# Kernel tuning notes

Measured on AMD Instinct MI355X. Metric: run time of the kernel, lower is better.

Reference implementation:

```python
import jax, jax.numpy as jnp
import numpy as np
from jax import lax

INPUT_SIZE, HIDDEN, LAYERS, OUT = 49, 32, 2, 10
B, T = 512, 1024


def _param(key, shape, fan):
    bound = 1.0 / np.sqrt(fan)
    return jax.random.uniform(key, shape, jnp.float32, -bound, bound)


def setup_inputs() -> dict:
    key = jax.random.key(0)
    ks = jax.random.split(key, 12)
    return {
        "x": jax.random.normal(ks[0], (B, T, INPUT_SIZE), jnp.float32),
        "W_ih0": _param(ks[1], (4 * HIDDEN, INPUT_SIZE), HIDDEN),
        "W_hh0": _param(ks[2], (4 * HIDDEN, HIDDEN), HIDDEN),
        "b_ih0": _param(ks[3], (4 * HIDDEN,), HIDDEN),
        "b_hh0": _param(ks[4], (4 * HIDDEN,), HIDDEN),
        "W_ih1": _param(ks[5], (4 * HIDDEN, HIDDEN), HIDDEN),
        "W_hh1": _param(ks[6], (4 * HIDDEN, HIDDEN), HIDDEN),
        "b_ih1": _param(ks[7], (4 * HIDDEN,), HIDDEN),
        "b_hh1": _param(ks[8], (4 * HIDDEN,), HIDDEN),
        "W_out": _param(ks[9], (OUT, HIDDEN), HIDDEN),
        "b_out": _param(ks[10], (OUT,), HIDDEN),
    }


def _lstm_layer(x_tbd, W_ih, W_hh, b_ih, b_hh):
    # x_tbd: [T, B, D]; PyTorch gate order i, f, g, o stacked along 4H.
    H = W_hh.shape[1]
    # Precompute input contribution for all timesteps in one GEMM.
    xg = jnp.einsum('tbd,gd->tbg', x_tbd, W_ih) + b_ih + b_hh  # [T, B, 4H]

    def step(carry, xg_t):
        h, c = carry
        gates = xg_t + h @ W_hh.T  # [B, 4H]
        i, f, g, o = jnp.split(gates, 4, axis=-1)
        i = jax.nn.sigmoid(i)
        f = jax.nn.sigmoid(f)
        g = jnp.tanh(g)
        o = jax.nn.sigmoid(o)
        c = f * c + i * g
        h = o * jnp.tanh(c)
        return (h, c), h

    Bsz = x_tbd.shape[1]
    init = (jnp.zeros((Bsz, H), x_tbd.dtype), jnp.zeros((Bsz, H), x_tbd.dtype))
    _, hs = lax.scan(step, init, xg)
    return hs  # [T, B, H]


def reference(x, W_ih0, W_hh0, b_ih0, b_hh0, W_ih1, W_hh1, b_ih1, b_hh1, W_out, b_out):
    # Eval-mode forward (inter-layer dropout disabled).
    xt = jnp.transpose(x, (1, 0, 2))  # [T, B, 49]
    h0 = _lstm_layer(xt, W_ih0, W_hh0, b_ih0, b_hh0)  # [T, B, 32]
    h1 = _lstm_layer(h0, W_ih1, W_hh1, b_ih1, b_hh1)  # [T, B, 32]
    r_out = jnp.transpose(h1, (1, 0, 2))  # [B, T, 32]
    return r_out @ W_out.T + b_out  # [B, T, 10]
```

## Files before the change

kernel.cpp:

```cpp
#include <hip/hip_runtime.h>
#include <cstddef>

#define TSTEPS 1024
#define NIN    49
#define HID    32
#define OUTD   10
#define XSTR   52
#define SUPERS 259

typedef float v2f __attribute__((ext_vector_type(2)));

template<int CTRL>
__device__ __forceinline__ float quad(float v) {
    return __int_as_float(__builtin_amdgcn_mov_dpp(__float_as_int(v), CTRL, 0xF, 0xF, true));
}
__device__ __forceinline__ float sigm(float x) {
    return __builtin_amdgcn_rcpf(1.f + __expf(-x));
}
__device__ __forceinline__ void pkfma(v2f& acc, v2f a, v2f b) {
    asm("v_pk_fma_f32 %0, %1, %2, %0" : "+v"(acc) : "v"(a), "v"(b));
}

#define LOADH2(BASE, H2)                                                     \
    v2f H2[8];                                                               \
    {                                                                        \
        const float4* hp_ = (const float4*)(BASE);                           \
        const float4 a_ = hp_[0], b_ = hp_[1], c_ = hp_[2], d_ = hp_[3];     \
        H2[0] = (v2f){a_.x, a_.y}; H2[1] = (v2f){a_.z, a_.w};                \
        H2[2] = (v2f){b_.x, b_.y}; H2[3] = (v2f){b_.z, b_.w};                \
        H2[4] = (v2f){c_.x, c_.y}; H2[5] = (v2f){c_.z, c_.w};                \
        H2[6] = (v2f){d_.x, d_.y}; H2[7] = (v2f){d_.z, d_.w};                \
    }

#define DOTPK(W2, H2, S0, S1, S2, S3)                                        \
    float S0, S1, S2, S3;                                                    \
    {                                                                        \
        v2f p0 = {0.f,0.f}, p1 = {0.f,0.f}, p2 = {0.f,0.f}, p3 = {0.f,0.f}; \
        _Pragma("unroll")                                                    \
        for (int m_ = 0; m_ < 8; ++m_) {                                     \
            pkfma(p0, W2[0][m_], H2[m_]);                                    \
            pkfma(p1, W2[1][m_], H2[m_]);                                    \
            pkfma(p2, W2[2][m_], H2[m_]);                                    \
            pkfma(p3, W2[3][m_], H2[m_]);                                    \
        }                                                                    \
        S0 = p0.x + p0.y; S1 = p1.x + p1.y;                                  \
        S2 = p2.x + p2.y; S3 = p3.x + p3.y;                                  \
        S0 += quad<0xB1>(S0); S1 += quad<0xB1>(S1);                          \
        S2 += quad<0xB1>(S2); S3 += quad<0xB1>(S3);                          \
    }

__device__ __forceinline__ float gate_act(float s0, float s1, float s2, float s3,
                                          int gp, float& c) {
    const float inA = gp ? s2 + s2 : s0;
    const float inB = gp ? s3 : s1;
    const float sA = sigm(inA);
    const float sB = sigm(inB);
    const float vA = gp ? fmaf(2.f, sA, -1.f) : sA;
    const float xA = quad<0xB1>(vA);
    const float xB = quad<0xB1>(sB);
    const float ig = gp ? xA : vA;
    const float fg = gp ? xB : sB;
    const float gg = gp ? vA : xA;
    const float og = gp ? sB : xB;
    c = fmaf(fg, c, ig * gg);
    return og * fmaf(2.f, sigm(c + c), -1.f);
}

extern "C" __global__ void __launch_bounds__(256, 2)
lstm_pk4(const float* __restrict__ x,
         const float* __restrict__ Wih0, const float* __restrict__ Whh0,
         const float* __restrict__ bih0, const float* __restrict__ bhh0,
         const float* __restrict__ Wih1, const float* __restrict__ Whh1,
         const float* __restrict__ bih1, const float* __restrict__ bhh1,
         const float* __restrict__ Wout, const float* __restrict__ bout,
         float* __restrict__ y)
{
    const int tid  = threadIdx.x;
    const int wv   = tid >> 6;
    const int lane = tid & 63;

    __shared__ float xs[2 * 16 * XSTR];
    __shared__ float xg0[16][HID][4];
    __shared__ float xg1[16][HID][4];
    __shared__ float h0r[16][HID];
    __shared__ float h1r[16][HID];

    {
        float* z0 = &h0r[0][0];
        float* z1 = &h1r[0][0];
        for (int i = tid; i < 16 * HID; i += 256) { z0[i] = 0.f; z1[i] = 0.f; }
    }

    const float* __restrict__ xb = x + (size_t)blockIdx.x * TSTEPS * NIN;
    float* __restrict__ yb       = y + (size_t)blockIdx.x * TSTEPS * OUTD;

    if (wv == 0) {
        const int j = lane >> 1, gp = lane & 1;
        v2f wh0[4][8];
#pragma unroll
        for (int g = 0; g < 4; ++g) {
            const float* wr = Whh0 + (g * HID + j) * HID + 16 * gp;
#pragma unroll
            for (int m = 0; m < 8; ++m) wh0[g][m] = (v2f){wr[2*m], wr[2*m + 1]};
        }
        float c0 = 0.f;
        __builtin_amdgcn_s_setprio(1);
        __syncthreads();
        __syncthreads();
        for (int s = 0; s < SUPERS; ++s) {
            if (s < 256) {
#pragma unroll
                for (int u = 0; u < 4; ++u) {
                    const int t = 4 * s + u;
                    LOADH2(&h0r[(t + 15) & 15][16 * gp], hv)
                    DOTPK(wh0, hv, s0, s1, s2, s3)
                    const float4 xg = *(const float4*)&xg0[t & 15][j][0];
                    const float hval = gate_act(s0 + xg.x, s1 + xg.y,
                                                s2 + xg.z, s3 + xg.w, gp, c0);
                    if (gp == 0) h0r[t & 15][j] = hval;
                }
            }
            __syncthreads();
        }
    } else if (wv == 1) {
        const int j = lane >> 1, gp = lane & 1;
        v2f wi1[4][8];
        float b1v[4];
#pragma unroll
        for (int g = 0; g < 4; ++g) {
            const float* wr = Wih1 + (g * HID + j) * HID + 16 * gp;
#pragma unroll
            for (int m = 0; m < 8; ++m) wi1[g][m] = (v2f){wr[2*m], wr[2*m + 1]};
            b1v[g] = bih1[g * HID + j] + bhh1[g * HID + j];
        }
        float wo[8], bo = 0.f;
        const int po = lane >> 2, kq = lane & 3;
        if (lane < 40) {
#pragma unroll
            for (int m = 0; m < 8; ++m) wo[m] = Wout[po * HID + kq * 8 + m];
            bo = bout[po];
        } else {
#pragma unroll
            for (int m = 0; m < 8; ++m) wo[m] = 0.f;
        }
        __syncthreads();
        __syncthreads();
        for (int s = 0; s < SUPERS; ++s) {
            if (s >= 1 && s <= 256) {
#pragma unroll
                for (int u = 0; u < 4; ++u) {
                    const int t = 4 * (s - 1) + u;
                    LOADH2(&h0r[t & 15][16 * gp], hv)
                    DOTPK(wi1, hv, s0, s1, s2, s3)
                    if (gp == 0) {
                        float4 o;
                        o.x = s0 + b1v[0]; o.y = s1 + b1v[1];
                        o.z = s2 + b1v[2]; o.w = s3 + b1v[3];
                        *(float4*)&xg1[t & 15][j][0] = o;
                    }
                }
            }
            if (s >= 3) {
#pragma unroll
                for (int u = 0; u < 4; ++u) {
                    const int ty = 4 * (s - 3) + u;
                    const float* hb = &h1r[ty & 15][kq * 8];
                    const float4 va = *(const float4*)hb;
                    const float4 vb = *(const float4*)(hb + 4);
                    float acc = wo[0]*va.x + wo[1]*va.y + wo[2]*va.z + wo[3]*va.w
                              + wo[4]*vb.x + wo[5]*vb.y + wo[6]*vb.z + wo[7]*vb.w;
                    acc += quad<0xB1>(acc);
                    acc += quad<0x4E>(acc);
                    if (lane < 40 && kq == 0) yb[(size_t)ty * OUTD + po] = acc + bo;
                }
            }
            __syncthreads();
        }
    } else if (wv == 2) {
        const int j = lane >> 1, gp = lane & 1;
        v2f wh1[4][8];
#pragma unroll
        for (int g = 0; g < 4; ++g) {
            const float* wr = Whh1 + (g * HID + j) * HID + 16 * gp;
#pragma unroll
            for (int m = 0; m < 8; ++m) wh1[g][m] = (v2f){wr[2*m], wr[2*m + 1]};
        }
        float c1 = 0.f;
        __builtin_amdgcn_s_setprio(1);
        __syncthreads();
        __syncthreads();
        for (int s = 0; s < SUPERS; ++s) {
            if (s >= 2 && s <= 257) {
#pragma unroll
                for (int u = 0; u < 4; ++u) {
                    const int t = 4 * (s - 2) + u;
                    LOADH2(&h1r[(t + 15) & 15][16 * gp], hv)
                    DOTPK(wh1, hv, s0, s1, s2, s3)
                    const float4 xg = *(const float4*)&xg1[t & 15][j][0];
                    const float hval = gate_act(s0 + xg.x, s1 + xg.y,
                                                s2 + xg.z, s3 + xg.w, gp, c1);
                    if (gp == 0) h1r[t & 15][j] = hval;
                }
            }
            __syncthreads();
        }
    } else {
        const int jj = lane & 31;
        const int gA = lane >> 5;
        const int gB = 2 + (lane >> 5);

        v2f wa2[24], wb2[24];
        float wa48, wb48, b0a, b0b;
        {
            const float* wra = Wih0 + (gA * HID + jj) * NIN;
            const float* wrb = Wih0 + (gB * HID + jj) * NIN;
#pragma unroll
            for (int m = 0; m < 24; ++m) {
                wa2[m] = (v2f){wra[2*m], wra[2*m + 1]};
                wb2[m] = (v2f){wrb[2*m], wrb[2*m + 1]};
            }
            wa48 = wra[48]; wb48 = wrb[48];
            b0a = bih0[gA * HID + jj] + bhh0[gA * HID + jj];
            b0b = bih0[gB * HID + jj] + bhh0[gB * HID + jj];
        }

        int laddr[13];
#pragma unroll
        for (int r = 0; r < 13; ++r) {
            const int idx = lane + r * 64;
            const int s_  = idx / NIN;
            laddr[r] = s_ * XSTR + (idx - s_ * NIN);
        }
        float xr[13];

        auto issue = [&](int cn) {
            const float* src = xb + (size_t)cn * 16 * NIN;
#pragma unroll
            for (int r = 0; r < 12; ++r) xr[r] = src[lane + r * 64];
            if (lane < 16) xr[12] = src[lane + 768];
        };
        auto drain = [&](int cn) {
            float* dst = &xs[(cn & 1) * (16 * XSTR)];
#pragma unroll
            for (int r = 0; r < 12; ++r) dst[laddr[r]] = xr[r];
            if (lane < 16) dst[laddr[12]] = xr[12];
        };
        auto pdot = [&](int t) {
            const float* xp = &xs[((t >> 4) & 1) * (16 * XSTR) + (t & 15) * XSTR];
            const float4* x4 = (const float4*)xp;
            v2f aA0 = (v2f){b0a, 0.f}, aA1 = (v2f){0.f, 0.f};
            v2f aB0 = (v2f){b0b, 0.f}, aB1 = (v2f){0.f, 0.f};
#pragma unroll
            for (int u = 0; u < 12; ++u) {
                const float4 xv = x4[u];
                const v2f xlo = (v2f){xv.x, xv.y};
                const v2f xhi = (v2f){xv.z, xv.w};
                pkfma(aA0, wa2[2*u],     xlo);
                pkfma(aA1, wa2[2*u + 1], xhi);
                pkfma(aB0, wb2[2*u],     xlo);
                pkfma(aB1, wb2[2*u + 1], xhi);
            }
            const float x48 = xp[48];
            const float a0 = fmaf(wa48, x48, (aA0.x + aA0.y) + (aA1.x + aA1.y));
            const float a2 = fmaf(wb48, x48, (aB0.x + aB0.y) + (aB1.x + aB1.y));
            xg0[t & 15][jj][gA] = a0;
            xg0[t & 15][jj][gB] = a2;
        };

        issue(0);
        drain(0);
        __syncthreads();
        pdot(0); pdot(1); pdot(2); pdot(3);
        __syncthreads();

        for (int s = 0; s < SUPERS; ++s) {
            if (s < 255) {
                const int cn = (s >> 2) + 1;
                if ((s & 3) == 0 && cn < 64) issue(cn);
                pdot(4 * s + 4); pdot(4 * s + 5); pdot(4 * s + 6); pdot(4 * s + 7);
                if ((s & 3) == 2 && cn < 64) drain(cn);
            }
            __syncthreads();
        }
    }
}

extern "C" void kernel_launch(void* const* d_in, const int* in_sizes, int n_in,
                              void* d_out, int out_size, void* d_ws, size_t ws_size,
                              hipStream_t stream) {
    (void)in_sizes; (void)n_in; (void)d_ws; (void)ws_size; (void)out_size;
    const float* x    = (const float*)d_in[0];
    const float* Wih0 = (const float*)d_in[1];
    const float* Whh0 = (const float*)d_in[2];
    const float* bih0 = (const float*)d_in[3];
    const float* bhh0 = (const float*)d_in[4];
    const float* Wih1 = (const float*)d_in[5];
    const float* Whh1 = (const float*)d_in[6];
    const float* bih1 = (const float*)d_in[7];
    const float* bhh1 = (const float*)d_in[8];
    const float* Wout = (const float*)d_in[9];
    const float* bout = (const float*)d_in[10];
    float* y = (float*)d_out;

    lstm_pk4<<<dim3(512), dim3(256), 0, stream>>>(
        x, Wih0, Whh0, bih0, bhh0, Wih1, Whh1, bih1, bhh1, Wout, bout, y);
}
```

Measured before the change: 400.4 us.

## Process two batch sequences per block to interleave independent recurrences

Each block now handles two batch rows instead of one. Every wave runs both recurrences side by side, so the independent dot products and gate activations can fill each other's latency on the serial critical path. The grid halves to 256 blocks and launch bounds drop to one block per SIMD group, so the GPU gets fewer blocks and lower occupancy. Register pressure roughly doubles for the x staging buffers and accumulators.

```diff
diff --git a/kernel.cpp b/kernel.cpp
--- a/kernel.cpp
+++ b/kernel.cpp
@@ -7,6 +7,7 @@
 #define OUTD   10
 #define XSTR   52
 #define SUPERS 259
+#define NB     2
 
 typedef float v2f __attribute__((ext_vector_type(2)));
 
@@ -32,21 +33,26 @@
         H2[6] = (v2f){d_.x, d_.y}; H2[7] = (v2f){d_.z, d_.w};                \
     }
 
-#define DOTPK(W2, H2, S0, S1, S2, S3)                                        \
-    float S0, S1, S2, S3;                                                    \
+#define DOTPK2(W2, HA, HB, A0,A1,A2,A3, B0,B1,B2,B3)                         \
+    float A0,A1,A2,A3,B0,B1,B2,B3;                                           \
     {                                                                        \
-        v2f p0 = {0.f,0.f}, p1 = {0.f,0.f}, p2 = {0.f,0.f}, p3 = {0.f,0.f}; \
+        v2f pa0={0.f,0.f}, pa1={0.f,0.f}, pa2={0.f,0.f}, pa3={0.f,0.f};      \
+        v2f pb0={0.f,0.f}, pb1={0.f,0.f}, pb2={0.f,0.f}, pb3={0.f,0.f};      \
         _Pragma("unroll")                                                    \
         for (int m_ = 0; m_ < 8; ++m_) {                                     \
-            pkfma(p0, W2[0][m_], H2[m_]);                                    \
-            pkfma(p1, W2[1][m_], H2[m_]);                                    \
-            pkfma(p2, W2[2][m_], H2[m_]);                                    \
-            pkfma(p3, W2[3][m_], H2[m_]);                                    \
+            pkfma(pa0, W2[0][m_], HA[m_]); pkfma(pb0, W2[0][m_], HB[m_]);    \
+            pkfma(pa1, W2[1][m_], HA[m_]); pkfma(pb1, W2[1][m_], HB[m_]);    \
+            pkfma(pa2, W2[2][m_], HA[m_]); pkfma(pb2, W2[2][m_], HB[m_]);    \
+            pkfma(pa3, W2[3][m_], HA[m_]); pkfma(pb3, W2[3][m_], HB[m_]);    \
         }                                                                    \
-        S0 = p0.x + p0.y; S1 = p1.x + p1.y;                                  \
-        S2 = p2.x + p2.y; S3 = p3.x + p3.y;                                  \
-        S0 += quad<0xB1>(S0); S1 += quad<0xB1>(S1);                          \
-        S2 += quad<0xB1>(S2); S3 += quad<0xB1>(S3);                          \
+        A0 = pa0.x + pa0.y; A1 = pa1.x + pa1.y;                              \
+        A2 = pa2.x + pa2.y; A3 = pa3.x + pa3.y;                              \
+        B0 = pb0.x + pb0.y; B1 = pb1.x + pb1.y;                              \
+        B2 = pb2.x + pb2.y; B3 = pb3.x + pb3.y;                              \
+        A0 += quad<0xB1>(A0); A1 += quad<0xB1>(A1);                          \
+        A2 += quad<0xB1>(A2); A3 += quad<0xB1>(A3);                          \
+        B0 += quad<0xB1>(B0); B1 += quad<0xB1>(B1);                          \
+        B2 += quad<0xB1>(B2); B3 += quad<0xB1>(B3);                          \
     }
 
 __device__ __forceinline__ float gate_act(float s0, float s1, float s2, float s3,
@@ -66,33 +72,35 @@
     return og * fmaf(2.f, sigm(c + c), -1.f);
 }
 
-extern "C" __global__ void __launch_bounds__(256, 2)
-lstm_pk4(const float* __restrict__ x,
-         const float* __restrict__ Wih0, const float* __restrict__ Whh0,
-         const float* __restrict__ bih0, const float* __restrict__ bhh0,
-         const float* __restrict__ Wih1, const float* __restrict__ Whh1,
-         const float* __restrict__ bih1, const float* __restrict__ bhh1,
-         const float* __restrict__ Wout, const float* __restrict__ bout,
-         float* __restrict__ y)
+extern "C" __global__ void __launch_bounds__(256, 1)
+lstm_pk4x2(const float* __restrict__ x,
+           const float* __restrict__ Wih0, const float* __restrict__ Whh0,
+           const float* __restrict__ bih0, const float* __restrict__ bhh0,
+           const float* __restrict__ Wih1, const float* __restrict__ Whh1,
+           const float* __restrict__ bih1, const float* __restrict__ bhh1,
+           const float* __restrict__ Wout, const float* __restrict__ bout,
+           float* __restrict__ y)
 {
     const int tid  = threadIdx.x;
     const int wv   = tid >> 6;
     const int lane = tid & 63;
 
-    __shared__ float xs[2 * 16 * XSTR];
-    __shared__ float xg0[16][HID][4];
-    __shared__ float xg1[16][HID][4];
-    __shared__ float h0r[16][HID];
-    __shared__ float h1r[16][HID];
+    __shared__ __align__(16) float xs[NB][2 * 16 * XSTR];
+    __shared__ __align__(16) float xg0[NB][16][HID][4];
+    __shared__ __align__(16) float xg1[NB][16][HID][4];
+    __shared__ __align__(16) float h0r[NB][16][HID];
+    __shared__ __align__(16) float h1r[NB][16][HID];
 
     {
-        float* z0 = &h0r[0][0];
-        float* z1 = &h1r[0][0];
-        for (int i = tid; i < 16 * HID; i += 256) { z0[i] = 0.f; z1[i] = 0.f; }
+        float* z0 = &h0r[0][0][0];
+        float* z1 = &h1r[0][0][0];
+        for (int i = tid; i < NB * 16 * HID; i += 256) { z0[i] = 0.f; z1[i] = 0.f; }
     }
 
-    const float* __restrict__ xb = x + (size_t)blockIdx.x * TSTEPS * NIN;
-    float* __restrict__ yb       = y + (size_t)blockIdx.x * TSTEPS * OUTD;
+    const float* __restrict__ xb0 = x + (size_t)blockIdx.x * NB * TSTEPS * NIN;
+    const float* __restrict__ xb1 = xb0 + TSTEPS * NIN;
+    float* __restrict__ yb0      = y + (size_t)blockIdx.x * NB * TSTEPS * OUTD;
+    float* __restrict__ yb1      = yb0 + TSTEPS * OUTD;
 
     if (wv == 0) {
         const int j = lane >> 1, gp = lane & 1;
@@ -103,7 +111,7 @@
 #pragma unroll
             for (int m = 0; m < 8; ++m) wh0[g][m] = (v2f){wr[2*m], wr[2*m + 1]};
         }
-        float c0 = 0.f;
+        float ca = 0.f, cb = 0.f;
         __builtin_amdgcn_s_setprio(1);
         __syncthreads();
         __syncthreads();
@@ -112,12 +120,19 @@
 #pragma unroll
                 for (int u = 0; u < 4; ++u) {
                     const int t = 4 * s + u;
-                    LOADH2(&h0r[(t + 15) & 15][16 * gp], hv)
-                    DOTPK(wh0, hv, s0, s1, s2, s3)
-                    const float4 xg = *(const float4*)&xg0[t & 15][j][0];
-                    const float hval = gate_act(s0 + xg.x, s1 + xg.y,
-                                                s2 + xg.z, s3 + xg.w, gp, c0);
-                    if (gp == 0) h0r[t & 15][j] = hval;
+                    LOADH2(&h0r[0][(t + 15) & 15][16 * gp], hva)
+                    LOADH2(&h0r[1][(t + 15) & 15][16 * gp], hvb)
+                    const float4 xga = *(const float4*)&xg0[0][t & 15][j][0];
+                    const float4 xgb = *(const float4*)&xg0[1][t & 15][j][0];
+                    DOTPK2(wh0, hva, hvb, a0, a1, a2, a3, b0, b1, b2, b3)
+                    const float ha = gate_act(a0 + xga.x, a1 + xga.y,
+                                              a2 + xga.z, a3 + xga.w, gp, ca);
+                    const float hb = gate_act(b0 + xgb.x, b1 + xgb.y,
+                                              b2 + xgb.z, b3 + xgb.w, gp, cb);
+                    if (gp == 0) {
+                        h0r[0][t & 15][j] = ha;
+                        h0r[1][t & 15][j] = hb;
+                    }
                 }
             }
             __syncthreads();
@@ -150,13 +165,17 @@
 #pragma unroll
                 for (int u = 0; u < 4; ++u) {
                     const int t = 4 * (s - 1) + u;
-                    LOADH2(&h0r[t & 15][16 * gp], hv)
-                    DOTPK(wi1, hv, s0, s1, s2, s3)
+                    LOADH2(&h0r[0][t & 15][16 * gp], hva)
+                    LOADH2(&h0r[1][t & 15][16 * gp], hvb)
+                    DOTPK2(wi1, hva, hvb, a0, a1, a2, a3, b0, b1, b2, b3)
                     if (gp == 0) {
-                        float4 o;
-                        o.x = s0 + b1v[0]; o.y = s1 + b1v[1];
-                        o.z = s2 + b1v[2]; o.w = s3 + b1v[3];
-                        *(float4*)&xg1[t & 15][j][0] = o;
+                        float4 oa, ob;
+                        oa.x = a0 + b1v[0]; oa.y = a1 + b1v[1];
+                        oa.z = a2 + b1v[2]; oa.w = a3 + b1v[3];
+                        ob.x = b0 + b1v[0]; ob.y = b1 + b1v[1];
+                        ob.z = b2 + b1v[2]; ob.w = b3 + b1v[3];
+                        *(float4*)&xg1[0][t & 15][j][0] = oa;
+                        *(float4*)&xg1[1][t & 15][j][0] = ob;
                     }
                 }
             }
@@ -164,14 +183,26 @@
 #pragma unroll
                 for (int u = 0; u < 4; ++u) {
                     const int ty = 4 * (s - 3) + u;
-                    const float* hb = &h1r[ty & 15][kq * 8];
-                    const float4 va = *(const float4*)hb;
-                    const float4 vb = *(const float4*)(hb + 4);
-                    float acc = wo[0]*va.x + wo[1]*va.y + wo[2]*va.z + wo[3]*va.w
-                              + wo[4]*vb.x + wo[5]*vb.y + wo[6]*vb.z + wo[7]*vb.w;
-                    acc += quad<0xB1>(acc);
-                    acc += quad<0x4E>(acc);
-                    if (lane < 40 && kq == 0) yb[(size_t)ty * OUTD + po] = acc + bo;
+                    {
+                        const float* hb = &h1r[0][ty & 15][kq * 8];
+                        const float4 va = *(const float4*)hb;
+                        const float4 vb = *(const float4*)(hb + 4);
+                        float acc = wo[0]*va.x + wo[1]*va.y + wo[2]*va.z + wo[3]*va.w
+                                  + wo[4]*vb.x + wo[5]*vb.y + wo[6]*vb.z + wo[7]*vb.w;
+                        acc += quad<0xB1>(acc);
+                        acc += quad<0x4E>(acc);
+                        if (lane < 40 && kq == 0) yb0[(size_t)ty * OUTD + po] = acc + bo;
+                    }
+                    {
+                        const float* hb = &h1r[1][ty & 15][kq * 8];
+                        const float4 va = *(const float4*)hb;
+                        const float4 vb = *(const float4*)(hb + 4);
+                        float acc = wo[0]*va.x + wo[1]*va.y + wo[2]*va.z + wo[3]*va.w
+                                  + wo[4]*vb.x + wo[5]*vb.y + wo[6]*vb.z + wo[7]*vb.w;
+                        acc += quad<0xB1>(acc);
+                        acc += quad<0x4E>(acc);
+                        if (lane < 40 && kq == 0) yb1[(size_t)ty * OUTD + po] = acc + bo;
+                    }
                 }
             }
             __syncthreads();
@@ -185,7 +216,7 @@
 #pragma unroll
             for (int m = 0; m < 8; ++m) wh1[g][m] = (v2f){wr[2*m], wr[2*m + 1]};
         }
-        float c1 = 0.f;
+        float ca = 0.f, cb = 0.f;
         __builtin_amdgcn_s_setprio(1);
         __syncthreads();
         __syncthreads();
@@ -194,12 +225,19 @@
 #pragma unroll
                 for (int u = 0; u < 4; ++u) {
                     const int t = 4 * (s - 2) + u;
-                    LOADH2(&h1r[(t + 15) & 15][16 * gp], hv)
-                    DOTPK(wh1, hv, s0, s1, s2, s3)
-                    const float4 xg = *(const float4*)&xg1[t & 15][j][0];
-                    const float hval = gate_act(s0 + xg.x, s1 + xg.y,
-                                                s2 + xg.z, s3 + xg.w, gp, c1);
-                    if (gp == 0) h1r[t & 15][j] = hval;
+                    LOADH2(&h1r[0][(t + 15) & 15][16 * gp], hva)
+                    LOADH2(&h1r[1][(t + 15) & 15][16 * gp], hvb)
+                    const float4 xga = *(const float4*)&xg1[0][t & 15][j][0];
+                    const float4 xgb = *(const float4*)&xg1[1][t & 15][j][0];
+                    DOTPK2(wh1, hva, hvb, a0, a1, a2, a3, b0, b1, b2, b3)
+                    const float ha = gate_act(a0 + xga.x, a1 + xga.y,
+                                              a2 + xga.z, a3 + xga.w, gp, ca);
+                    const float hb = gate_act(b0 + xgb.x, b1 + xgb.y,
+                                              b2 + xgb.z, b3 + xgb.w, gp, cb);
+                    if (gp == 0) {
+                        h1r[0][t & 15][j] = ha;
+                        h1r[1][t & 15][j] = hb;
+                    }
                 }
             }
             __syncthreads();
@@ -231,22 +269,30 @@
             const int s_  = idx / NIN;
             laddr[r] = s_ * XSTR + (idx - s_ * NIN);
         }
-        float xr[13];
+        float xra[13], xrb[13];
 
         auto issue = [&](int cn) {
-            const float* src = xb + (size_t)cn * 16 * NIN;
-#pragma unroll
-            for (int r = 0; r < 12; ++r) xr[r] = src[lane + r * 64];
-            if (lane < 16) xr[12] = src[lane + 768];
+            const float* sa = xb0 + (size_t)cn * 16 * NIN;
+            const float* sb = xb1 + (size_t)cn * 16 * NIN;
+#pragma unroll
+            for (int r = 0; r < 12; ++r) {
+                xra[r] = sa[lane + r * 64];
+                xrb[r] = sb[lane + r * 64];
+            }
+            if (lane < 16) { xra[12] = sa[lane + 768]; xrb[12] = sb[lane + 768]; }
         };
         auto drain = [&](int cn) {
-            float* dst = &xs[(cn & 1) * (16 * XSTR)];
-#pragma unroll
-            for (int r = 0; r < 12; ++r) dst[laddr[r]] = xr[r];
-            if (lane < 16) dst[laddr[12]] = xr[12];
+            float* da = &xs[0][(cn & 1) * (16 * XSTR)];
+            float* db = &xs[1][(cn & 1) * (16 * XSTR)];
+#pragma unroll
+            for (int r = 0; r < 12; ++r) {
+                da[laddr[r]] = xra[r];
+                db[laddr[r]] = xrb[r];
+            }
+            if (lane < 16) { da[laddr[12]] = xra[12]; db[laddr[12]] = xrb[12]; }
         };
-        auto pdot = [&](int t) {
-            const float* xp = &xs[((t >> 4) & 1) * (16 * XSTR) + (t & 15) * XSTR];
+        auto pdot1 = [&](int t, int b) {
+            const float* xp = &xs[b][((t >> 4) & 1) * (16 * XSTR) + (t & 15) * XSTR];
             const float4* x4 = (const float4*)xp;
             v2f aA0 = (v2f){b0a, 0.f}, aA1 = (v2f){0.f, 0.f};
             v2f aB0 = (v2f){b0b, 0.f}, aB1 = (v2f){0.f, 0.f};
@@ -263,21 +309,25 @@
             const float x48 = xp[48];
             const float a0 = fmaf(wa48, x48, (aA0.x + aA0.y) + (aA1.x + aA1.y));
             const float a2 = fmaf(wb48, x48, (aB0.x + aB0.y) + (aB1.x + aB1.y));
-            xg0[t & 15][jj][gA] = a0;
-            xg0[t & 15][jj][gB] = a2;
+            xg0[b][t & 15][jj][gA] = a0;
+            xg0[b][t & 15][jj][gB] = a2;
         };
 
         issue(0);
         drain(0);
         __syncthreads();
-        pdot(0); pdot(1); pdot(2); pdot(3);
+        pdot1(0, 0); pdot1(0, 1); pdot1(1, 0); pdot1(1, 1);
+        pdot1(2, 0); pdot1(2, 1); pdot1(3, 0); pdot1(3, 1);
         __syncthreads();
 
         for (int s = 0; s < SUPERS; ++s) {
             if (s < 255) {
                 const int cn = (s >> 2) + 1;
                 if ((s & 3) == 0 && cn < 64) issue(cn);
-                pdot(4 * s + 4); pdot(4 * s + 5); pdot(4 * s + 6); pdot(4 * s + 7);
+                pdot1(4 * s + 4, 0); pdot1(4 * s + 4, 1);
+                pdot1(4 * s + 5, 0); pdot1(4 * s + 5, 1);
+                pdot1(4 * s + 6, 0); pdot1(4 * s + 6, 1);
+                pdot1(4 * s + 7, 0); pdot1(4 * s + 7, 1);
                 if ((s & 3) == 2 && cn < 64) drain(cn);
             }
             __syncthreads();
@@ -302,6 +352,6 @@
     const float* bout = (const float*)d_in[10];
     float* y = (float*)d_out;
 
-    lstm_pk4<<<dim3(512), dim3(256), 0, stream>>>(
+    lstm_pk4x2<<<dim3(512 / NB), dim3(256), 0, stream>>>(
         x, Wih0, Whh0, bih0, bhh0, Wih1, Whh1, bih1, bhh1, Wout, bout, y);
 }
```

Result: slower. 546.4 us (+36.5%).

## Fuse LSTM wave roles into two waves per block with interleaved work

Applied to the files above, without the earlier changes.

Merges the four specialized waves into two. One wave runs the layer-0 recurrence, the layer-1 input projection and the output projection. The other runs the layer-0 input projection and the layer-1 recurrence. In steady state the independent work is interleaved within each timestep so it can fill the latency gaps of the serial recurrence, and the block shrinks to 128 threads. The risk is a longer per-wave instruction stream on the critical path, plus the loss of the priority boost that was previously given to the recurrence waves.

```diff
diff --git a/kernel.cpp b/kernel.cpp
--- a/kernel.cpp
+++ b/kernel.cpp
@@ -66,29 +66,29 @@
     return og * fmaf(2.f, sigm(c + c), -1.f);
 }
 
-extern "C" __global__ void __launch_bounds__(256, 2)
-lstm_pk4(const float* __restrict__ x,
-         const float* __restrict__ Wih0, const float* __restrict__ Whh0,
-         const float* __restrict__ bih0, const float* __restrict__ bhh0,
-         const float* __restrict__ Wih1, const float* __restrict__ Whh1,
-         const float* __restrict__ bih1, const float* __restrict__ bhh1,
-         const float* __restrict__ Wout, const float* __restrict__ bout,
-         float* __restrict__ y)
+extern "C" __global__ void __launch_bounds__(128, 2)
+lstm_fuse2(const float* __restrict__ x,
+           const float* __restrict__ Wih0, const float* __restrict__ Whh0,
+           const float* __restrict__ bih0, const float* __restrict__ bhh0,
+           const float* __restrict__ Wih1, const float* __restrict__ Whh1,
+           const float* __restrict__ bih1, const float* __restrict__ bhh1,
+           const float* __restrict__ Wout, const float* __restrict__ bout,
+           float* __restrict__ y)
 {
     const int tid  = threadIdx.x;
     const int wv   = tid >> 6;
     const int lane = tid & 63;
 
-    __shared__ float xs[2 * 16 * XSTR];
-    __shared__ float xg0[16][HID][4];
-    __shared__ float xg1[16][HID][4];
-    __shared__ float h0r[16][HID];
-    __shared__ float h1r[16][HID];
+    __shared__ __align__(16) float xs[2 * 16 * XSTR];
+    __shared__ __align__(16) float xg0[16][HID][4];
+    __shared__ __align__(16) float xg1[16][HID][4];
+    __shared__ __align__(16) float h0r[16][HID];
+    __shared__ __align__(16) float h1r[16][HID];
 
     {
         float* z0 = &h0r[0][0];
         float* z1 = &h1r[0][0];
-        for (int i = tid; i < 16 * HID; i += 256) { z0[i] = 0.f; z1[i] = 0.f; }
+        for (int i = tid; i < 16 * HID; i += 128) { z0[i] = 0.f; z1[i] = 0.f; }
     }
 
     const float* __restrict__ xb = x + (size_t)blockIdx.x * TSTEPS * NIN;
@@ -96,74 +96,52 @@
 
     if (wv == 0) {
         const int j = lane >> 1, gp = lane & 1;
-        v2f wh0[4][8];
+        v2f wh0[4][8], wi1[4][8];
+        float b1v[4];
 #pragma unroll
         for (int g = 0; g < 4; ++g) {
-            const float* wr = Whh0 + (g * HID + j) * HID + 16 * gp;
-#pragma unroll
-            for (int m = 0; m < 8; ++m) wh0[g][m] = (v2f){wr[2*m], wr[2*m + 1]};
+            const float* wr0 = Whh0 + (g * HID + j) * HID + 16 * gp;
+            const float* wr1 = Wih1 + (g * HID + j) * HID + 16 * gp;
+#pragma unroll
+            for (int m = 0; m < 8; ++m) {
+                wh0[g][m] = (v2f){wr0[2*m], wr0[2*m + 1]};
+                wi1[g][m] = (v2f){wr1[2*m], wr1[2*m + 1]};
+            }
+            b1v[g] = bih1[g * HID + j] + bhh1[g * HID + j];
+        }
+        float wo[8], bo = 0.f;
+        const int po = lane >> 2, kq = lane & 3;
+        if (lane < 40) {
+#pragma unroll
+            for (int m = 0; m < 8; ++m) wo[m] = Wout[po * HID + kq * 8 + m];
+            bo = bout[po];
+        } else {
+#pragma unroll
+            for (int m = 0; m < 8; ++m) wo[m] = 0.f;
         }
         float c0 = 0.f;
-        __builtin_amdgcn_s_setprio(1);
         __syncthreads();
         __syncthreads();
         for (int s = 0; s < SUPERS; ++s) {
-            if (s < 256) {
+            if (s >= 3 && s < 256) {
 #pragma unroll
                 for (int u = 0; u < 4; ++u) {
                     const int t = 4 * s + u;
+                    LOADH2(&h0r[(t - 4) & 15][16 * gp], hq)
                     LOADH2(&h0r[(t + 15) & 15][16 * gp], hv)
+                    const float4 xg = *(const float4*)&xg0[t & 15][j][0];
                     DOTPK(wh0, hv, s0, s1, s2, s3)
-                    const float4 xg = *(const float4*)&xg0[t & 15][j][0];
+                    DOTPK(wi1, hq, q0, q1, q2, q3)
                     const float hval = gate_act(s0 + xg.x, s1 + xg.y,
                                                 s2 + xg.z, s3 + xg.w, gp, c0);
-                    if (gp == 0) h0r[t & 15][j] = hval;
-                }
-            }
-            __syncthreads();
-        }
-    } else if (wv == 1) {
-        const int j = lane >> 1, gp = lane & 1;
-        v2f wi1[4][8];
-        float b1v[4];
-#pragma unroll
-        for (int g = 0; g < 4; ++g) {
-            const float* wr = Wih1 + (g * HID + j) * HID + 16 * gp;
-#pragma unroll
-            for (int m = 0; m < 8; ++m) wi1[g][m] = (v2f){wr[2*m], wr[2*m + 1]};
-            b1v[g] = bih1[g * HID + j] + bhh1[g * HID + j];
-        }
-        float wo[8], bo = 0.f;
-        const int po = lane >> 2, kq = lane & 3;
-        if (lane < 40) {
-#pragma unroll
-            for (int m = 0; m < 8; ++m) wo[m] = Wout[po * HID + kq * 8 + m];
-            bo = bout[po];
-        } else {
-#pragma unroll
-            for (int m = 0; m < 8; ++m) wo[m] = 0.f;
-        }
-        __syncthreads();
-        __syncthreads();
-        for (int s = 0; s < SUPERS; ++s) {
-            if (s >= 1 && s <= 256) {
-#pragma unroll
-                for (int u = 0; u < 4; ++u) {
-                    const int t = 4 * (s - 1) + u;
-                    LOADH2(&h0r[t & 15][16 * gp], hv)
-                    DOTPK(wi1, hv, s0, s1, s2, s3)
                     if (gp == 0) {
+                        h0r[t & 15][j] = hval;
                         float4 o;
-                        o.x = s0 + b1v[0]; o.y = s1 + b1v[1];
-                        o.z = s2 + b1v[2]; o.w = s3 + b1v[3];
-                        *(float4*)&xg1[t & 15][j][0] = o;
-                    }
-                }
-            }
-            if (s >= 3) {
-#pragma unroll
-                for (int u = 0; u < 4; ++u) {
-                    const int ty = 4 * (s - 3) + u;
+                        o.x = q0 + b1v[0]; o.y = q1 + b1v[1];
+                        o.z = q2 + b1v[2]; o.w = q3 + b1v[3];
+                        *(float4*)&xg1[(t - 4) & 15][j][0] = o;
+                    }
+                    const int ty = t - 12;
                     const float* hb = &h1r[ty & 15][kq * 8];
                     const float4 va = *(const float4*)hb;
                     const float4 vb = *(const float4*)(hb + 4);
@@ -173,10 +151,51 @@
                     acc += quad<0x4E>(acc);
                     if (lane < 40 && kq == 0) yb[(size_t)ty * OUTD + po] = acc + bo;
                 }
+            } else {
+                if (s < 256) {
+#pragma unroll
+                    for (int u = 0; u < 4; ++u) {
+                        const int t = 4 * s + u;
+                        LOADH2(&h0r[(t + 15) & 15][16 * gp], hv)
+                        DOTPK(wh0, hv, s0, s1, s2, s3)
+                        const float4 xg = *(const float4*)&xg0[t & 15][j][0];
+                        const float hval = gate_act(s0 + xg.x, s1 + xg.y,
+                                                    s2 + xg.z, s3 + xg.w, gp, c0);
+                        if (gp == 0) h0r[t & 15][j] = hval;
+                    }
+                }
+                if (s >= 1 && s <= 256) {
+#pragma unroll
+                    for (int u = 0; u < 4; ++u) {
+                        const int tq = 4 * (s - 1) + u;
+                        LOADH2(&h0r[tq & 15][16 * gp], hq)
+                        DOTPK(wi1, hq, q0, q1, q2, q3)
+                        if (gp == 0) {
+                            float4 o;
+                            o.x = q0 + b1v[0]; o.y = q1 + b1v[1];
+                            o.z = q2 + b1v[2]; o.w = q3 + b1v[3];
+                            *(float4*)&xg1[tq & 15][j][0] = o;
+                        }
+                    }
+                }
+                if (s >= 3) {
+#pragma unroll
+                    for (int u = 0; u < 4; ++u) {
+                        const int ty = 4 * (s - 3) + u;
+                        const float* hb = &h1r[ty & 15][kq * 8];
+                        const float4 va = *(const float4*)hb;
+                        const float4 vb = *(const float4*)(hb + 4);
+                        float acc = wo[0]*va.x + wo[1]*va.y + wo[2]*va.z + wo[3]*va.w
+                                  + wo[4]*vb.x + wo[5]*vb.y + wo[6]*vb.z + wo[7]*vb.w;
+                        acc += quad<0xB1>(acc);
+                        acc += quad<0x4E>(acc);
+                        if (lane < 40 && kq == 0) yb[(size_t)ty * OUTD + po] = acc + bo;
+                    }
+                }
             }
             __syncthreads();
         }
-    } else if (wv == 2) {
+    } else {
         const int j = lane >> 1, gp = lane & 1;
         v2f wh1[4][8];
 #pragma unroll
@@ -185,30 +204,9 @@
 #pragma unroll
             for (int m = 0; m < 8; ++m) wh1[g][m] = (v2f){wr[2*m], wr[2*m + 1]};
         }
-        float c1 = 0.f;
-        __builtin_amdgcn_s_setprio(1);
-        __syncthreads();
-        __syncthreads();
-        for (int s = 0; s < SUPERS; ++s) {
-            if (s >= 2 && s <= 257) {
-#pragma unroll
-                for (int u = 0; u < 4; ++u) {
-                    const int t = 4 * (s - 2) + u;
-                    LOADH2(&h1r[(t + 15) & 15][16 * gp], hv)
-                    DOTPK(wh1, hv, s0, s1, s2, s3)
-                    const float4 xg = *(const float4*)&xg1[t & 15][j][0];
-                    const float hval = gate_act(s0 + xg.x, s1 + xg.y,
-                                                s2 + xg.z, s3 + xg.w, gp, c1);
-                    if (gp == 0) h1r[t & 15][j] = hval;
-                }
-            }
-            __syncthreads();
-        }
-    } else {
         const int jj = lane & 31;
         const int gA = lane >> 5;
         const int gB = 2 + (lane >> 5);
-
         v2f wa2[24], wb2[24];
         float wa48, wb48, b0a, b0b;
         {
@@ -267,6 +265,8 @@
             xg0[t & 15][jj][gB] = a2;
         };
 
+        float c1 = 0.f;
+
         issue(0);
         drain(0);
         __syncthreads();
@@ -274,11 +274,40 @@
         __syncthreads();
 
         for (int s = 0; s < SUPERS; ++s) {
-            if (s < 255) {
+            if (s >= 2 && s < 255) {
                 const int cn = (s >> 2) + 1;
                 if ((s & 3) == 0 && cn < 64) issue(cn);
-                pdot(4 * s + 4); pdot(4 * s + 5); pdot(4 * s + 6); pdot(4 * s + 7);
+#pragma unroll
+                for (int u = 0; u < 4; ++u) {
+                    const int t = 4 * (s - 2) + u;
+                    LOADH2(&h1r[(t + 15) & 15][16 * gp], hv)
+                    const float4 xg = *(const float4*)&xg1[t & 15][j][0];
+                    DOTPK(wh1, hv, s0, s1, s2, s3)
+                    const float hval = gate_act(s0 + xg.x, s1 + xg.y,
+                                                s2 + xg.z, s3 + xg.w, gp, c1);
+                    if (gp == 0) h1r[t & 15][j] = hval;
+                    pdot(4 * (s + 1) + u);
+                }
                 if ((s & 3) == 2 && cn < 64) drain(cn);
+            } else {
+                if (s < 255) {
+                    const int cn = (s >> 2) + 1;
+                    if ((s & 3) == 0 && cn < 64) issue(cn);
+                    pdot(4 * s + 4); pdot(4 * s + 5); pdot(4 * s + 6); pdot(4 * s + 7);
+                    if ((s & 3) == 2 && cn < 64) drain(cn);
+                }
+                if (s >= 2 && s <= 257) {
+#pragma unroll
+                    for (int u = 0; u < 4; ++u) {
+                        const int t = 4 * (s - 2) + u;
+                        LOADH2(&h1r[(t + 15) & 15][16 * gp], hv)
+                        const float4 xg = *(const float4*)&xg1[t & 15][j][0];
+                        DOTPK(wh1, hv, s0, s1, s2, s3)
+                        const float hval = gate_act(s0 + xg.x, s1 + xg.y,
+                                                    s2 + xg.z, s3 + xg.w, gp, c1);
+                        if (gp == 0) h1r[t & 15][j] = hval;
+                    }
+                }
             }
             __syncthreads();
         }
@@ -302,6 +331,6 @@
     const float* bout = (const float*)d_in[10];
     float* y = (float*)d_out;
 
-    lstm_pk4<<<dim3(512), dim3(256), 0, stream>>>(
+    lstm_fuse2<<<dim3(512), dim3(128), 0, stream>>>(
         x, Wih0, Whh0, bih0, bhh0, Wih1, Whh1, bih1, bhh1, Wout, bout, y);
 }
```

Measured after the change: 671.0 us. 67.6% more time.

## Replace block-wide barriers with per-stage LDS counter flags between warp roles

Applied to the files above, without the earlier changes.

Removes the lockstep __syncthreads per super-step and has each wavefront role (input projection, layer-0 recurrence, layer-1 input GEMM/output projection, layer-1 recurrence) publish progress through release-stores to shared counters, while consumers spin with acquire loads and s_sleep. This lets the stages drift within the 16-slot ring buffers so the slowest wave no longer stalls all four at every step. It adds polling overhead and relies on the ring-distance checks being correct for memory ordering.

```diff
diff --git a/kernel.cpp b/kernel.cpp
--- a/kernel.cpp
+++ b/kernel.cpp
@@ -6,7 +6,7 @@
 #define HID    32
 #define OUTD   10
 #define XSTR   52
-#define SUPERS 259
+#define NGRP   256
 
 typedef float v2f __attribute__((ext_vector_type(2)));
 
@@ -19,6 +19,20 @@
 }
 __device__ __forceinline__ void pkfma(v2f& acc, v2f a, v2f b) {
     asm("v_pk_fma_f32 %0, %1, %2, %0" : "+v"(acc) : "v"(a), "v"(b));
+}
+
+__device__ __forceinline__ int ldacq(const int* p) {
+    return __hip_atomic_load(p, __ATOMIC_ACQUIRE, __HIP_MEMORY_SCOPE_WORKGROUP);
+}
+__device__ __forceinline__ void pub(int* p, int v, int lane) {
+    if (lane == 0)
+        __hip_atomic_store(p, v, __ATOMIC_RELEASE, __HIP_MEMORY_SCOPE_WORKGROUP);
+}
+__device__ __forceinline__ void waitge(const int* p, int need, int& cache) {
+    if (cache >= need) return;
+    int c = ldacq(p);
+    while (c < need) { __builtin_amdgcn_s_sleep(1); c = ldacq(p); }
+    cache = c;
 }
 
 #define LOADH2(BASE, H2)                                                     \
@@ -67,29 +81,32 @@
 }
 
 extern "C" __global__ void __launch_bounds__(256, 2)
-lstm_pk4(const float* __restrict__ x,
-         const float* __restrict__ Wih0, const float* __restrict__ Whh0,
-         const float* __restrict__ bih0, const float* __restrict__ bhh0,
-         const float* __restrict__ Wih1, const float* __restrict__ Whh1,
-         const float* __restrict__ bih1, const float* __restrict__ bhh1,
-         const float* __restrict__ Wout, const float* __restrict__ bout,
-         float* __restrict__ y)
+lstm_async(const float* __restrict__ x,
+           const float* __restrict__ Wih0, const float* __restrict__ Whh0,
+           const float* __restrict__ bih0, const float* __restrict__ bhh0,
+           const float* __restrict__ Wih1, const float* __restrict__ Whh1,
+           const float* __restrict__ bih1, const float* __restrict__ bhh1,
+           const float* __restrict__ Wout, const float* __restrict__ bout,
+           float* __restrict__ y)
 {
     const int tid  = threadIdx.x;
     const int wv   = tid >> 6;
     const int lane = tid & 63;
 
-    __shared__ float xs[2 * 16 * XSTR];
-    __shared__ float xg0[16][HID][4];
-    __shared__ float xg1[16][HID][4];
-    __shared__ float h0r[16][HID];
-    __shared__ float h1r[16][HID];
+    __shared__ __align__(16) float xs[2 * 16 * XSTR];
+    __shared__ __align__(16) float xg0[16][HID][4];
+    __shared__ __align__(16) float xg1[16][HID][4];
+    __shared__ __align__(16) float h0r[16][HID];
+    __shared__ __align__(16) float h1r[16][HID];
+    __shared__ int ctr[5];
 
     {
         float* z0 = &h0r[0][0];
         float* z1 = &h1r[0][0];
         for (int i = tid; i < 16 * HID; i += 256) { z0[i] = 0.f; z1[i] = 0.f; }
+        if (tid < 5) ctr[tid] = -1;
     }
+    __syncthreads();
 
     const float* __restrict__ xb = x + (size_t)blockIdx.x * TSTEPS * NIN;
     float* __restrict__ yb       = y + (size_t)blockIdx.x * TSTEPS * OUTD;
@@ -104,23 +121,22 @@
             for (int m = 0; m < 8; ++m) wh0[g][m] = (v2f){wr[2*m], wr[2*m + 1]};
         }
         float c0 = 0.f;
+        int cProd = -1, cQd = -1;
         __builtin_amdgcn_s_setprio(1);
-        __syncthreads();
-        __syncthreads();
-        for (int s = 0; s < SUPERS; ++s) {
-            if (s < 256) {
-#pragma unroll
-                for (int u = 0; u < 4; ++u) {
-                    const int t = 4 * s + u;
-                    LOADH2(&h0r[(t + 15) & 15][16 * gp], hv)
-                    DOTPK(wh0, hv, s0, s1, s2, s3)
-                    const float4 xg = *(const float4*)&xg0[t & 15][j][0];
-                    const float hval = gate_act(s0 + xg.x, s1 + xg.y,
-                                                s2 + xg.z, s3 + xg.w, gp, c0);
-                    if (gp == 0) h0r[t & 15][j] = hval;
-                }
-            }
-            __syncthreads();
+        for (int g = 0; g < NGRP; ++g) {
+            waitge(&ctr[0], 4 * g + 3, cProd);
+            if (g >= 4) waitge(&ctr[2], 4 * g - 13, cQd);
+#pragma unroll
+            for (int u = 0; u < 4; ++u) {
+                const int t = 4 * g + u;
+                LOADH2(&h0r[(t + 15) & 15][16 * gp], hv)
+                DOTPK(wh0, hv, s0, s1, s2, s3)
+                const float4 xg = *(const float4*)&xg0[t & 15][j][0];
+                const float hval = gate_act(s0 + xg.x, s1 + xg.y,
+                                            s2 + xg.z, s3 + xg.w, gp, c0);
+                if (gp == 0) h0r[t & 15][j] = hval;
+            }
+            pub(&ctr[1], 4 * g + 3, lane);
         }
     } else if (wv == 1) {
         const int j = lane >> 1, gp = lane & 1;
@@ -143,27 +159,31 @@
 #pragma unroll
             for (int m = 0; m < 8; ++m) wo[m] = 0.f;
         }
-        __syncthreads();
-        __syncthreads();
-        for (int s = 0; s < SUPERS; ++s) {
-            if (s >= 1 && s <= 256) {
+        int cL0 = -1, cL1b = -1, cL1d = -1;
+        for (int g = 0; g < NGRP + 2; ++g) {
+            if (g < NGRP) {
+                waitge(&ctr[1], 4 * g + 3, cL0);
+                if (g >= 4) waitge(&ctr[3], 4 * g - 13, cL1b);
 #pragma unroll
                 for (int u = 0; u < 4; ++u) {
-                    const int t = 4 * (s - 1) + u;
-                    LOADH2(&h0r[t & 15][16 * gp], hv)
-                    DOTPK(wi1, hv, s0, s1, s2, s3)
+                    const int t = 4 * g + u;
+                    LOADH2(&h0r[t & 15][16 * gp], hq)
+                    DOTPK(wi1, hq, q0, q1, q2, q3)
                     if (gp == 0) {
                         float4 o;
-                        o.x = s0 + b1v[0]; o.y = s1 + b1v[1];
-                        o.z = s2 + b1v[2]; o.w = s3 + b1v[3];
+                        o.x = q0 + b1v[0]; o.y = q1 + b1v[1];
+                        o.z = q2 + b1v[2]; o.w = q3 + b1v[3];
                         *(float4*)&xg1[t & 15][j][0] = o;
                     }
                 }
-            }
-            if (s >= 3) {
+                pub(&ctr[2], 4 * g + 3, lane);
+            }
+            if (g >= 2) {
+                const int gy = g - 2;
+                waitge(&ctr[3], 4 * gy + 3, cL1d);
 #pragma unroll
                 for (int u = 0; u < 4; ++u) {
-                    const int ty = 4 * (s - 3) + u;
+                    const int ty = 4 * gy + u;
                     const float* hb = &h1r[ty & 15][kq * 8];
                     const float4 va = *(const float4*)hb;
                     const float4 vb = *(const float4*)(hb + 4);
@@ -173,8 +193,8 @@
                     acc += quad<0x4E>(acc);
                     if (lane < 40 && kq == 0) yb[(size_t)ty * OUTD + po] = acc + bo;
                 }
-            }
-            __syncthreads();
+                pub(&ctr[4], 4 * gy + 3, lane);
+            }
         }
     } else if (wv == 2) {
         const int j = lane >> 1, gp = lane & 1;
@@ -186,23 +206,22 @@
             for (int m = 0; m < 8; ++m) wh1[g][m] = (v2f){wr[2*m], wr[2*m + 1]};
         }
         float c1 = 0.f;
+        int cQd = -1, cPrj = -1;
         __builtin_amdgcn_s_setprio(1);
-        __syncthreads();
-        __syncthreads();
-        for (int s = 0; s < SUPERS; ++s) {
-            if (s >= 2 && s <= 257) {
-#pragma unroll
-                for (int u = 0; u < 4; ++u) {
-                    const int t = 4 * (s - 2) + u;
-                    LOADH2(&h1r[(t + 15) & 15][16 * gp], hv)
-                    DOTPK(wh1, hv, s0, s1, s2, s3)
-                    const float4 xg = *(const float4*)&xg1[t & 15][j][0];
-                    const float hval = gate_act(s0 + xg.x, s1 + xg.y,
-                                                s2 + xg.z, s3 + xg.w, gp, c1);
-                    if (gp == 0) h1r[t & 15][j] = hval;
-                }
-            }
-            __syncthreads();
+        for (int g = 0; g < NGRP; ++g) {
+            waitge(&ctr[2], 4 * g + 3, cQd);
+            if (g >= 4) waitge(&ctr[4], 4 * g - 13, cPrj);
+#pragma unroll
+            for (int u = 0; u < 4; ++u) {
+                const int t = 4 * g + u;
+                LOADH2(&h1r[(t + 15) & 15][16 * gp], hv)
+                DOTPK(wh1, hv, s0, s1, s2, s3)
+                const float4 xg = *(const float4*)&xg1[t & 15][j][0];
+                const float hval = gate_act(s0 + xg.x, s1 + xg.y,
+                                            s2 + xg.z, s3 + xg.w, gp, c1);
+                if (gp == 0) h1r[t & 15][j] = hval;
+            }
+            pub(&ctr[3], 4 * g + 3, lane);
         }
     } else {
         const int jj = lane & 31;
@@ -269,18 +288,15 @@
 
         issue(0);
         drain(0);
-        __syncthreads();
-        pdot(0); pdot(1); pdot(2); pdot(3);
-        __syncthreads();
-
-        for (int s = 0; s < SUPERS; ++s) {
-            if (s < 255) {
-                const int cn = (s >> 2) + 1;
-                if ((s & 3) == 0 && cn < 64) issue(cn);
-                pdot(4 * s + 4); pdot(4 * s + 5); pdot(4 * s + 6); pdot(4 * s + 7);
-                if ((s & 3) == 2 && cn < 64) drain(cn);
-            }
-            __syncthreads();
+
+        int cL0 = -1;
+        for (int g = 0; g < NGRP; ++g) {
+            if (g >= 4) waitge(&ctr[1], 4 * g - 13, cL0);
+            const int cn = (g >> 2) + 1;
+            if ((g & 3) == 0 && cn < 64) issue(cn);
+            pdot(4 * g); pdot(4 * g + 1); pdot(4 * g + 2); pdot(4 * g + 3);
+            if ((g & 3) == 2 && cn < 64) drain(cn);
+            pub(&ctr[0], 4 * g + 3, lane);
         }
     }
 }
@@ -302,6 +318,6 @@
     const float* bout = (const float*)d_in[10];
     float* y = (float*)d_out;
 
-    lstm_pk4<<<dim3(512), dim3(256), 0, stream>>>(
+    lstm_async<<<dim3(512), dim3(256), 0, stream>>>(
         x, Wih0, Whh0, bih0, bhh0, Wih1, Whh1, bih1, bhh1, Wout, bout, y);
 }
```

After: 400.3 us. Within noise of the previous version (-0.0%).
